# Kernel tuning notes

Measured on AMD Instinct MI355X. Metric: run time of the kernel, lower is better.

Reference implementation:

```python
import jax, jax.numpy as jnp
import numpy as np

N_NODES = 100000
N_EDGES = 1280000
IN_CH = 64
OUT_CH = 64


def setup_inputs() -> dict:
    key = jax.random.key(0)
    k1, k2, k3, k4 = jax.random.split(key, 4)
    x = jax.random.normal(k1, (N_NODES, IN_CH), dtype=jnp.float32)
    edge_index = jax.random.randint(k2, (2, N_EDGES), 0, N_NODES, dtype=jnp.int64)
    # GraphConv params (glorot weight, zero bias)
    scale = jnp.sqrt(6.0 / (IN_CH + OUT_CH)).astype(jnp.float32)
    W = jax.random.uniform(k3, (IN_CH, OUT_CH), dtype=jnp.float32, minval=-scale, maxval=scale)
    b = jnp.zeros((OUT_CH,), dtype=jnp.float32)
    return {"x": x, "edge_index": edge_index, "W": W, "b": b}


def reference(x, edge_index, W, b):
    # DGL GraphConv, norm='both': out = D_in^{-1/2} A^T (D_out^{-1/2} x W) + b
    src, dst = edge_index[0], edge_index[1]
    ones = jnp.ones((src.shape[0],), dtype=x.dtype)
    out_deg = jax.ops.segment_sum(ones, src, num_segments=N_NODES)
    in_deg = jax.ops.segment_sum(ones, dst, num_segments=N_NODES)
    norm_src = jnp.where(out_deg > 0, jax.lax.rsqrt(jnp.maximum(out_deg, 1.0)), 0.0)
    norm_dst = jnp.where(in_deg > 0, jax.lax.rsqrt(jnp.maximum(in_deg, 1.0)), 0.0)
    # in_feats <= out_feats: transform first, then aggregate
    h = (x * norm_src[:, None]) @ W              # [N, OUT_CH]
    msg = h[src]                                 # gather  [E, OUT_CH]
    agg = jax.ops.segment_sum(msg, dst, num_segments=N_NODES)  # scatter-add [N, OUT_CH]
    return agg * norm_dst[:, None] + b
```

## Files before the change

kernel.cpp:

```cpp
#include <hip/hip_runtime.h>
#include <hip/hip_fp16.h>

#define CH 64
#define CAP 40
#define SPILLMAX 4096
#define RANGE 12500
#define SLICES 64
#define TILE 2048
#define EPT 8
#define BSH 9
#define BKT 512

__global__ __launch_bounds__(256) void hist_kernel(const int* __restrict__ src,
                                                   unsigned short* __restrict__ partial,
                                                   int E, int N, int R)
{
    __shared__ int h[RANGE];
    int r  = blockIdx.x % R;
    int sl = blockIdx.x / R;
    int lo = r * RANGE;
    int hi = min(lo + RANGE, N);
    int span = hi - lo;
    for (int i = threadIdx.x; i < span; i += 256) h[i] = 0;
    __syncthreads();
    int per = (E + SLICES - 1) / SLICES;
    int sb = sl * per, se = min(sb + per, E);
    for (int e = sb + threadIdx.x * 4; e < se; e += 256 * 4) {
        if (e + 4 <= se) {
            int4 v = *(const int4*)(src + e);
            if (v.x >= lo && v.x < hi) atomicAdd(&h[v.x - lo], 1);
            if (v.y >= lo && v.y < hi) atomicAdd(&h[v.y - lo], 1);
            if (v.z >= lo && v.z < hi) atomicAdd(&h[v.z - lo], 1);
            if (v.w >= lo && v.w < hi) atomicAdd(&h[v.w - lo], 1);
        } else {
            for (int k = e; k < se; ++k) {
                int sv = src[k];
                if (sv >= lo && sv < hi) atomicAdd(&h[sv - lo], 1);
            }
        }
    }
    __syncthreads();
    unsigned short* pp = partial + (size_t)blockIdx.x * RANGE;
    for (int i = threadIdx.x; i < span; i += 256) pp[i] = (unsigned short)h[i];
}

__global__ __launch_bounds__(256) void rpscale_kernel(const unsigned short* __restrict__ partial,
                                                      const float* __restrict__ x,
                                                      __half* __restrict__ xh, int N, int R)
{
    __shared__ float nsl[256];
    int tid = threadIdx.x;
    int n0 = blockIdx.x * 256;
    int n = n0 + tid;
    if (n < N) {
        int r = n / RANGE, off = n - r * RANGE;
        int s = 0;
        #pragma unroll 8
        for (int sl = 0; sl < SLICES; ++sl)
            s += partial[(size_t)(sl * R + r) * RANGE + off];
        nsl[tid] = (s > 0) ? rsqrtf((float)s) : 0.0f;
    } else {
        nsl[tid] = 0.0f;
    }
    __syncthreads();
    int sub = tid & 7;
    int nl0 = tid >> 3;
    for (int p = 0; p < 8; ++p) {
        int nl = p * 32 + nl0;
        int node = n0 + nl;
        if (node >= N) break;
        float ns = nsl[nl];
        const float4* xp = (const float4*)(x + (size_t)node * CH + sub * 8);
        float4 a = xp[0], b = xp[1];
        __half2 h0 = __floats2half2_rn(a.x * ns, a.y * ns);
        __half2 h1 = __floats2half2_rn(a.z * ns, a.w * ns);
        __half2 h2 = __floats2half2_rn(b.x * ns, b.y * ns);
        __half2 h3 = __floats2half2_rn(b.z * ns, b.w * ns);
        uint4 u;
        u.x = (unsigned)__half_as_ushort(h0.x) | ((unsigned)__half_as_ushort(h0.y) << 16);
        u.y = (unsigned)__half_as_ushort(h1.x) | ((unsigned)__half_as_ushort(h1.y) << 16);
        u.z = (unsigned)__half_as_ushort(h2.x) | ((unsigned)__half_as_ushort(h2.y) << 16);
        u.w = (unsigned)__half_as_ushort(h3.x) | ((unsigned)__half_as_ushort(h3.y) << 16);
        *(uint4*)(xh + (size_t)node * CH + sub * 8) = u;
    }
}

__global__ __launch_bounds__(256) void binA_kernel(const int* __restrict__ dst,
                                                   int* __restrict__ tileHist,
                                                   int* __restrict__ nspill, int E)
{
    if (blockIdx.x == 0 && threadIdx.x == 0) nspill[0] = 0;
    __shared__ int h[256];
    int tid = threadIdx.x;
    int t = blockIdx.x;
    h[tid] = 0;
    __syncthreads();
    int e0 = t * TILE + tid * EPT;
    if (e0 + EPT <= E) {
        const int4* dp = (const int4*)(dst + e0);
        int4 a = dp[0], b = dp[1];
        atomicAdd(&h[a.x >> BSH], 1); atomicAdd(&h[a.y >> BSH], 1);
        atomicAdd(&h[a.z >> BSH], 1); atomicAdd(&h[a.w >> BSH], 1);
        atomicAdd(&h[b.x >> BSH], 1); atomicAdd(&h[b.y >> BSH], 1);
        atomicAdd(&h[b.z >> BSH], 1); atomicAdd(&h[b.w >> BSH], 1);
    } else {
        for (int k = e0; k < E && k < e0 + EPT; ++k) atomicAdd(&h[dst[k] >> BSH], 1);
    }
    __syncthreads();
    tileHist[t * 256 + tid] = h[tid];
}

__global__ __launch_bounds__(256) void binB_kernel(int* __restrict__ tileHist,
                                                   int* __restrict__ totals, int NT)
{
    __shared__ int sm[256];
    int b = blockIdx.x, tid = threadIdx.x;
    int C = (NT + 255) / 256;
    int vals[8];
    int s = 0;
    for (int k = 0; k < C; ++k) {
        int t = tid * C + k;
        vals[k] = (t < NT) ? tileHist[t * 256 + b] : 0;
        s += vals[k];
    }
    sm[tid] = s;
    __syncthreads();
    for (int d = 1; d < 256; d <<= 1) {
        int v = (tid >= d) ? sm[tid - d] : 0;
        __syncthreads();
        sm[tid] += v;
        __syncthreads();
    }
    int off = (tid > 0) ? sm[tid - 1] : 0;
    for (int k = 0; k < C; ++k) {
        int t = tid * C + k;
        if (t < NT) { tileHist[t * 256 + b] = off; off += vals[k]; }
    }
    if (tid == 255) totals[b] = sm[255];
}

__global__ __launch_bounds__(256) void binC_kernel(const int* __restrict__ src,
                                                   const int* __restrict__ dst,
                                                   const int* __restrict__ tileBase,
                                                   const int* __restrict__ totals,
                                                   int* __restrict__ sorted, int E, int NB)
{
    __shared__ int sm[256];
    __shared__ int cur[256];
    int tid = threadIdx.x;
    int t = blockIdx.x;
    sm[tid] = (tid < NB) ? totals[tid] : 0;
    __syncthreads();
    for (int d = 1; d < 256; d <<= 1) {
        int v = (tid >= d) ? sm[tid - d] : 0;
        __syncthreads();
        sm[tid] += v;
        __syncthreads();
    }
    int bb = (tid > 0) ? sm[tid - 1] : 0;
    cur[tid] = (tid < NB) ? bb + tileBase[t * 256 + tid] : 0;
    __syncthreads();
    int e0 = t * TILE + tid * EPT;
    int s[EPT], d[EPT];
    int nk = 0;
    if (e0 + EPT <= E) {
        const int4* sp = (const int4*)(src + e0);
        const int4* dp = (const int4*)(dst + e0);
        int4 a = sp[0], b = sp[1], c = dp[0], f = dp[1];
        s[0]=a.x; s[1]=a.y; s[2]=a.z; s[3]=a.w; s[4]=b.x; s[5]=b.y; s[6]=b.z; s[7]=b.w;
        d[0]=c.x; d[1]=c.y; d[2]=c.z; d[3]=c.w; d[4]=f.x; d[5]=f.y; d[6]=f.z; d[7]=f.w;
        nk = EPT;
    } else {
        for (int k = 0; e0 + k < E && k < EPT; ++k) { s[k] = src[e0+k]; d[k] = dst[e0+k]; nk++; }
    }
    for (int k = 0; k < nk; ++k) {
        int p = d[k] >> BSH;
        int pos = atomicAdd(&cur[p], 1);
        sorted[pos] = (s[k] << BSH) | (d[k] & (BKT - 1));
    }
}

__global__ __launch_bounds__(256) void binD_kernel(const int* __restrict__ sorted,
                                                   const int* __restrict__ totals,
                                                   int* __restrict__ bucket,
                                                   int* __restrict__ cnt,
                                                   int* __restrict__ spill,
                                                   int* __restrict__ nspill, int N, int NB)
{
    __shared__ int sm[256];
    __shared__ int lc[BKT];
    int b = blockIdx.x, tid = threadIdx.x;
    sm[tid] = (tid < NB) ? totals[tid] : 0;
    lc[tid] = 0; lc[tid + 256] = 0;
    __syncthreads();
    for (int d = 1; d < 256; d <<= 1) {
        int v = (tid >= d) ? sm[tid - d] : 0;
        __syncthreads();
        sm[tid] += v;
        __syncthreads();
    }
    int beg = (b > 0) ? sm[b - 1] : 0;
    int end = sm[b];
    int nbase = b << BSH;
    for (int i = beg + tid; i < end; i += 256) {
        int v = sorted[i];
        int sv = v >> BSH;
        int dl = v & (BKT - 1);
        int pos = atomicAdd(&lc[dl], 1);
        if (pos < CAP) {
            bucket[(size_t)(nbase + dl) * CAP + pos] = sv;
        } else {
            int sp = atomicAdd(nspill, 1);
            if (sp < SPILLMAX) { spill[2*sp] = nbase + dl; spill[2*sp+1] = sv; }
        }
    }
    __syncthreads();
    int n0 = nbase + tid;
    if (n0 < N) cnt[n0] = lc[tid];
    int n1 = nbase + 256 + tid;
    if (n1 < N) cnt[n1] = lc[256 + tid];
}

__global__ __launch_bounds__(256) void agg_kernel(const __half* __restrict__ xh,
                                                  const int* __restrict__ bucket,
                                                  const int* __restrict__ cnt,
                                                  const int* __restrict__ spill,
                                                  const int* __restrict__ nspill,
                                                  __half* __restrict__ aggh, int N)
{
    int node = (blockIdx.x * blockDim.x + threadIdx.x) >> 5;
    int sl = threadIdx.x & 31;
    if (node >= N) return;
    int c = cnt[node];
    int m = (c < CAP) ? c : CAP;
    const int* bp = bucket + (size_t)node * CAP;
    float ax0 = 0, ay0 = 0, ax1 = 0, ay1 = 0, ax2 = 0, ay2 = 0, ax3 = 0, ay3 = 0;
    int j = 0;
    for (; j + 8 <= m; j += 8) {
        int4 va = *(const int4*)(bp + j);
        int4 vb = *(const int4*)(bp + j + 4);
        float2 f0 = __half22float2(*(const __half2*)(xh + (size_t)va.x * CH + sl * 2));
        float2 f1 = __half22float2(*(const __half2*)(xh + (size_t)va.y * CH + sl * 2));
        float2 f2 = __half22float2(*(const __half2*)(xh + (size_t)va.z * CH + sl * 2));
        float2 f3 = __half22float2(*(const __half2*)(xh + (size_t)va.w * CH + sl * 2));
        float2 f4 = __half22float2(*(const __half2*)(xh + (size_t)vb.x * CH + sl * 2));
        float2 f5 = __half22float2(*(const __half2*)(xh + (size_t)vb.y * CH + sl * 2));
        float2 f6 = __half22float2(*(const __half2*)(xh + (size_t)vb.z * CH + sl * 2));
        float2 f7 = __half22float2(*(const __half2*)(xh + (size_t)vb.w * CH + sl * 2));
        ax0 += f0.x + f4.x; ay0 += f0.y + f4.y;
        ax1 += f1.x + f5.x; ay1 += f1.y + f5.y;
        ax2 += f2.x + f6.x; ay2 += f2.y + f6.y;
        ax3 += f3.x + f7.x; ay3 += f3.y + f7.y;
    }
    for (; j + 4 <= m; j += 4) {
        int4 va = *(const int4*)(bp + j);
        float2 f0 = __half22float2(*(const __half2*)(xh + (size_t)va.x * CH + sl * 2));
        float2 f1 = __half22float2(*(const __half2*)(xh + (size_t)va.y * CH + sl * 2));
        float2 f2 = __half22float2(*(const __half2*)(xh + (size_t)va.z * CH + sl * 2));
        float2 f3 = __half22float2(*(const __half2*)(xh + (size_t)va.w * CH + sl * 2));
        ax0 += f0.x; ay0 += f0.y;
        ax1 += f1.x; ay1 += f1.y;
        ax2 += f2.x; ay2 += f2.y;
        ax3 += f3.x; ay3 += f3.y;
    }
    for (; j < m; ++j) {
        float2 f = __half22float2(*(const __half2*)(xh + (size_t)bp[j] * CH + sl * 2));
        ax0 += f.x; ay0 += f.y;
    }
    if (c > CAP) {
        int ns = *nspill;
        if (ns > SPILLMAX) ns = SPILLMAX;
        for (int i = 0; i < ns; ++i) {
            if (spill[2 * i] == node) {
                float2 f = __half22float2(*(const __half2*)(xh + (size_t)spill[2 * i + 1] * CH + sl * 2));
                ax0 += f.x; ay0 += f.y;
            }
        }
    }
    float nd = (c > 0) ? rsqrtf((float)c) : 0.0f;
    float rx = ((ax0 + ax1) + (ax2 + ax3)) * nd;
    float ry = ((ay0 + ay1) + (ay2 + ay3)) * nd;
    *(__half2*)(aggh + (size_t)node * CH + sl * 2) = __floats2half2_rn(rx, ry);
}

__global__ __launch_bounds__(256) void gemm_out_kernel(const __half* __restrict__ aggh,
                                                       const float* __restrict__ W,
                                                       const float* __restrict__ bias,
                                                       float* __restrict__ out, int N)
{
    int g = blockIdx.x * 256 + threadIdx.x;
    int waveId = __builtin_amdgcn_readfirstlane(g >> 6);
    int lane = threadIdx.x & 63;
    int quarter = waveId & 3;
    int row = ((waveId >> 2) << 6) + lane;
    if (row >= N) return;
    const int cbase = quarter * 16;
    float acc[16];
    #pragma unroll
    for (int i = 0; i < 16; ++i) acc[i] = 0.0f;
    const __half* xp = aggh + (size_t)row * CH;
    for (int k0 = 0; k0 < CH; k0 += 8) {
        uint4 u = *(const uint4*)(xp + k0);
        const __half2* hp = (const __half2*)&u;
        float xk[8];
        #pragma unroll
        for (int j = 0; j < 4; ++j) {
            float2 f = __half22float2(hp[j]);
            xk[2 * j] = f.x; xk[2 * j + 1] = f.y;
        }
        #pragma unroll
        for (int kk = 0; kk < 8; ++kk) {
            const float* wrow = W + (k0 + kk) * CH + cbase;
            #pragma unroll
            for (int q = 0; q < 4; ++q) {
                float4 w = *(const float4*)(wrow + q * 4);
                acc[q * 4 + 0] += xk[kk] * w.x;
                acc[q * 4 + 1] += xk[kk] * w.y;
                acc[q * 4 + 2] += xk[kk] * w.z;
                acc[q * 4 + 3] += xk[kk] * w.w;
            }
        }
    }
    float* op = out + (size_t)row * CH + cbase;
    #pragma unroll
    for (int q = 0; q < 4; ++q) {
        float4 b = *(const float4*)(bias + cbase + q * 4);
        float4 o;
        o.x = acc[q * 4 + 0] + b.x;
        o.y = acc[q * 4 + 1] + b.y;
        o.z = acc[q * 4 + 2] + b.z;
        o.w = acc[q * 4 + 3] + b.w;
        *(float4*)(op + q * 4) = o;
    }
}

extern "C" void kernel_launch(void* const* d_in, const int* in_sizes, int n_in,
                              void* d_out, int out_size, void* d_ws, size_t ws_size,
                              hipStream_t stream)
{
    const float* x    = (const float*)d_in[0];
    const int*   edge = (const int*)d_in[1];
    const float* W    = (const float*)d_in[2];
    const float* bias = (const float*)d_in[3];
    float* out = (float*)d_out;

    int N = in_sizes[0] / CH;
    int E = in_sizes[1] / 2;
    const int* src = edge;
    const int* dst = edge + E;
    int R  = (N + RANGE - 1) / RANGE;
    int NT = (E + TILE - 1) / TILE;
    int NB = (N + BKT - 1) >> BSH;

    int* nspill  = (int*)d_ws;
    int* spill   = nspill + 64;
    int* cnt     = spill + 2 * SPILLMAX;
    int* bucket  = cnt + N;
    unsigned short* partial = (unsigned short*)(bucket + (size_t)N * CAP);
    int* tileHist = (int*)partial;
    int* totals   = tileHist + NT * 256;
    int* sorted   = totals + 320;
    size_t psz = (size_t)SLICES * R * RANGE * sizeof(unsigned short);
    size_t osz = (size_t)(NT * 256 + 320 + E) * sizeof(int);
    size_t xoff = ((((char*)partial - (char*)d_ws) + (psz > osz ? psz : osz)) + 255) & ~(size_t)255;
    __half* xh = (__half*)((char*)d_ws + xoff);
    size_t aoff = ((xoff + (size_t)N * CH * sizeof(__half)) + 255) & ~(size_t)255;
    __half* aggh = (__half*)((char*)d_ws + aoff);

    hist_kernel<<<R * SLICES, 256, 0, stream>>>(src, partial, E, N, R);
    rpscale_kernel<<<(N + 255) / 256, 256, 0, stream>>>(partial, x, xh, N, R);
    binA_kernel<<<NT, 256, 0, stream>>>(dst, tileHist, nspill, E);
    binB_kernel<<<NB, 256, 0, stream>>>(tileHist, totals, NT);
    binC_kernel<<<NT, 256, 0, stream>>>(src, dst, tileHist, totals, sorted, E, NB);
    binD_kernel<<<NB, 256, 0, stream>>>(sorted, totals, bucket, cnt, spill, nspill, N, NB);
    agg_kernel<<<((size_t)N * 32 + 255) / 256, 256, 0, stream>>>(xh, bucket, cnt, spill,
                                                                 nspill, aggh, N);
    int nwaves = 4 * ((N + 63) / 64);
    gemm_out_kernel<<<(nwaves + 3) / 4, 256, 0, stream>>>(aggh, W, bias, out, N);
}
```

Before: 114.0 us.

## Merge histogram and binning kernels into combined launches via block-index dispatch

Combines the source-degree histogram with the destination tile histogram into one launch, and the rpscale/normalisation kernel with the bucket prefix-scan kernel into another, dispatching on block index. This removes two kernel launches and lets independent work run concurrently on the GPU. The workspace layout is reorganised so tileHist no longer aliases the partial buffer, and CAP shrinks from 40 to 32, which may push more nodes into the spill path. The tile-histogram blocks now allocate the large 12500-int shared array, which can reduce occupancy for those blocks.

```diff
diff --git a/kernel.cpp b/kernel.cpp
--- a/kernel.cpp
+++ b/kernel.cpp
@@ -2,7 +2,7 @@
 #include <hip/hip_fp16.h>
 
 #define CH 64
-#define CAP 40
+#define CAP 32
 #define SPILLMAX 4096
 #define RANGE 12500
 #define SLICES 64
@@ -11,132 +11,134 @@
 #define BSH 9
 #define BKT 512
 
-__global__ __launch_bounds__(256) void hist_kernel(const int* __restrict__ src,
-                                                   unsigned short* __restrict__ partial,
-                                                   int E, int N, int R)
+__global__ __launch_bounds__(256) void histA_kernel(const int* __restrict__ src,
+                                                    const int* __restrict__ dst,
+                                                    unsigned short* __restrict__ partial,
+                                                    int* __restrict__ tileHist,
+                                                    int* __restrict__ nspill,
+                                                    int E, int N, int R, int NT)
 {
     __shared__ int h[RANGE];
-    int r  = blockIdx.x % R;
-    int sl = blockIdx.x / R;
-    int lo = r * RANGE;
-    int hi = min(lo + RANGE, N);
-    int span = hi - lo;
-    for (int i = threadIdx.x; i < span; i += 256) h[i] = 0;
-    __syncthreads();
-    int per = (E + SLICES - 1) / SLICES;
-    int sb = sl * per, se = min(sb + per, E);
-    for (int e = sb + threadIdx.x * 4; e < se; e += 256 * 4) {
-        if (e + 4 <= se) {
-            int4 v = *(const int4*)(src + e);
-            if (v.x >= lo && v.x < hi) atomicAdd(&h[v.x - lo], 1);
-            if (v.y >= lo && v.y < hi) atomicAdd(&h[v.y - lo], 1);
-            if (v.z >= lo && v.z < hi) atomicAdd(&h[v.z - lo], 1);
-            if (v.w >= lo && v.w < hi) atomicAdd(&h[v.w - lo], 1);
+    int tid = threadIdx.x;
+    int bid = blockIdx.x;
+    if (bid < NT) {
+        if (bid == 0 && tid == 0) nspill[0] = 0;
+        h[tid] = 0;
+        __syncthreads();
+        int e0 = bid * TILE + tid * EPT;
+        if (e0 + EPT <= E) {
+            const int4* dp = (const int4*)(dst + e0);
+            int4 a = dp[0], b = dp[1];
+            atomicAdd(&h[a.x >> BSH], 1); atomicAdd(&h[a.y >> BSH], 1);
+            atomicAdd(&h[a.z >> BSH], 1); atomicAdd(&h[a.w >> BSH], 1);
+            atomicAdd(&h[b.x >> BSH], 1); atomicAdd(&h[b.y >> BSH], 1);
+            atomicAdd(&h[b.z >> BSH], 1); atomicAdd(&h[b.w >> BSH], 1);
         } else {
-            for (int k = e; k < se; ++k) {
-                int sv = src[k];
-                if (sv >= lo && sv < hi) atomicAdd(&h[sv - lo], 1);
+            for (int k = e0; k < E && k < e0 + EPT; ++k) atomicAdd(&h[dst[k] >> BSH], 1);
+        }
+        __syncthreads();
+        tileHist[bid * 256 + tid] = h[tid];
+    } else {
+        int hb = bid - NT;
+        int r  = hb % R;
+        int sl = hb / R;
+        int lo = r * RANGE;
+        int hi = min(lo + RANGE, N);
+        int span = hi - lo;
+        for (int i = tid; i < span; i += 256) h[i] = 0;
+        __syncthreads();
+        int per = (E + SLICES - 1) / SLICES;
+        int sb = sl * per, se = min(sb + per, E);
+        for (int e = sb + tid * 4; e < se; e += 256 * 4) {
+            if (e + 4 <= se) {
+                int4 v = *(const int4*)(src + e);
+                if (v.x >= lo && v.x < hi) atomicAdd(&h[v.x - lo], 1);
+                if (v.y >= lo && v.y < hi) atomicAdd(&h[v.y - lo], 1);
+                if (v.z >= lo && v.z < hi) atomicAdd(&h[v.z - lo], 1);
+                if (v.w >= lo && v.w < hi) atomicAdd(&h[v.w - lo], 1);
+            } else {
+                for (int k = e; k < se; ++k) {
+                    int sv = src[k];
+                    if (sv >= lo && sv < hi) atomicAdd(&h[sv - lo], 1);
+                }
             }
         }
-    }
-    __syncthreads();
-    unsigned short* pp = partial + (size_t)blockIdx.x * RANGE;
-    for (int i = threadIdx.x; i < span; i += 256) pp[i] = (unsigned short)h[i];
-}
-
-__global__ __launch_bounds__(256) void rpscale_kernel(const unsigned short* __restrict__ partial,
-                                                      const float* __restrict__ x,
-                                                      __half* __restrict__ xh, int N, int R)
+        __syncthreads();
+        unsigned short* pp = partial + (size_t)hb * RANGE;
+        for (int i = tid; i < span; i += 256) pp[i] = (unsigned short)h[i];
+    }
+}
+
+__global__ __launch_bounds__(256) void rpscaleB_kernel(const unsigned short* __restrict__ partial,
+                                                       const float* __restrict__ x,
+                                                       __half* __restrict__ xh,
+                                                       int* __restrict__ tileHist,
+                                                       int* __restrict__ totals,
+                                                       int N, int R, int NT, int NPB)
 {
     __shared__ float nsl[256];
+    __shared__ int sm[256];
     int tid = threadIdx.x;
-    int n0 = blockIdx.x * 256;
-    int n = n0 + tid;
-    if (n < N) {
-        int r = n / RANGE, off = n - r * RANGE;
+    int bid = blockIdx.x;
+    if (bid < NPB) {
+        int n0 = bid * 256;
+        int n = n0 + tid;
+        if (n < N) {
+            int r = n / RANGE, off = n - r * RANGE;
+            int s = 0;
+            #pragma unroll 8
+            for (int sl = 0; sl < SLICES; ++sl)
+                s += partial[(size_t)(sl * R + r) * RANGE + off];
+            nsl[tid] = (s > 0) ? rsqrtf((float)s) : 0.0f;
+        } else {
+            nsl[tid] = 0.0f;
+        }
+        __syncthreads();
+        int sub = tid & 7;
+        int nl0 = tid >> 3;
+        for (int p = 0; p < 8; ++p) {
+            int nl = p * 32 + nl0;
+            int node = n0 + nl;
+            if (node >= N) break;
+            float ns = nsl[nl];
+            const float4* xp = (const float4*)(x + (size_t)node * CH + sub * 8);
+            float4 a = xp[0], b = xp[1];
+            __half2 h0 = __floats2half2_rn(a.x * ns, a.y * ns);
+            __half2 h1 = __floats2half2_rn(a.z * ns, a.w * ns);
+            __half2 h2 = __floats2half2_rn(b.x * ns, b.y * ns);
+            __half2 h3 = __floats2half2_rn(b.z * ns, b.w * ns);
+            uint4 u;
+            u.x = (unsigned)__half_as_ushort(h0.x) | ((unsigned)__half_as_ushort(h0.y) << 16);
+            u.y = (unsigned)__half_as_ushort(h1.x) | ((unsigned)__half_as_ushort(h1.y) << 16);
+            u.z = (unsigned)__half_as_ushort(h2.x) | ((unsigned)__half_as_ushort(h2.y) << 16);
+            u.w = (unsigned)__half_as_ushort(h3.x) | ((unsigned)__half_as_ushort(h3.y) << 16);
+            *(uint4*)(xh + (size_t)node * CH + sub * 8) = u;
+        }
+    } else {
+        int b = bid - NPB;
+        int C = (NT + 255) / 256;
+        int vals[8];
         int s = 0;
-        #pragma unroll 8
-        for (int sl = 0; sl < SLICES; ++sl)
-            s += partial[(size_t)(sl * R + r) * RANGE + off];
-        nsl[tid] = (s > 0) ? rsqrtf((float)s) : 0.0f;
-    } else {
-        nsl[tid] = 0.0f;
-    }
-    __syncthreads();
-    int sub = tid & 7;
-    int nl0 = tid >> 3;
-    for (int p = 0; p < 8; ++p) {
-        int nl = p * 32 + nl0;
-        int node = n0 + nl;
-        if (node >= N) break;
-        float ns = nsl[nl];
-        const float4* xp = (const float4*)(x + (size_t)node * CH + sub * 8);
-        float4 a = xp[0], b = xp[1];
-        __half2 h0 = __floats2half2_rn(a.x * ns, a.y * ns);
-        __half2 h1 = __floats2half2_rn(a.z * ns, a.w * ns);
-        __half2 h2 = __floats2half2_rn(b.x * ns, b.y * ns);
-        __half2 h3 = __floats2half2_rn(b.z * ns, b.w * ns);
-        uint4 u;
-        u.x = (unsigned)__half_as_ushort(h0.x) | ((unsigned)__half_as_ushort(h0.y) << 16);
-        u.y = (unsigned)__half_as_ushort(h1.x) | ((unsigned)__half_as_ushort(h1.y) << 16);
-        u.z = (unsigned)__half_as_ushort(h2.x) | ((unsigned)__half_as_ushort(h2.y) << 16);
-        u.w = (unsigned)__half_as_ushort(h3.x) | ((unsigned)__half_as_ushort(h3.y) << 16);
-        *(uint4*)(xh + (size_t)node * CH + sub * 8) = u;
-    }
-}
-
-__global__ __launch_bounds__(256) void binA_kernel(const int* __restrict__ dst,
-                                                   int* __restrict__ tileHist,
-                                                   int* __restrict__ nspill, int E)
-{
-    if (blockIdx.x == 0 && threadIdx.x == 0) nspill[0] = 0;
-    __shared__ int h[256];
-    int tid = threadIdx.x;
-    int t = blockIdx.x;
-    h[tid] = 0;
-    __syncthreads();
-    int e0 = t * TILE + tid * EPT;
-    if (e0 + EPT <= E) {
-        const int4* dp = (const int4*)(dst + e0);
-        int4 a = dp[0], b = dp[1];
-        atomicAdd(&h[a.x >> BSH], 1); atomicAdd(&h[a.y >> BSH], 1);
-        atomicAdd(&h[a.z >> BSH], 1); atomicAdd(&h[a.w >> BSH], 1);
-        atomicAdd(&h[b.x >> BSH], 1); atomicAdd(&h[b.y >> BSH], 1);
-        atomicAdd(&h[b.z >> BSH], 1); atomicAdd(&h[b.w >> BSH], 1);
-    } else {
-        for (int k = e0; k < E && k < e0 + EPT; ++k) atomicAdd(&h[dst[k] >> BSH], 1);
-    }
-    __syncthreads();
-    tileHist[t * 256 + tid] = h[tid];
-}
-
-__global__ __launch_bounds__(256) void binB_kernel(int* __restrict__ tileHist,
-                                                   int* __restrict__ totals, int NT)
-{
-    __shared__ int sm[256];
-    int b = blockIdx.x, tid = threadIdx.x;
-    int C = (NT + 255) / 256;
-    int vals[8];
-    int s = 0;
-    for (int k = 0; k < C; ++k) {
-        int t = tid * C + k;
-        vals[k] = (t < NT) ? tileHist[t * 256 + b] : 0;
-        s += vals[k];
-    }
-    sm[tid] = s;
-    __syncthreads();
-    for (int d = 1; d < 256; d <<= 1) {
-        int v = (tid >= d) ? sm[tid - d] : 0;
-        __syncthreads();
-        sm[tid] += v;
-        __syncthreads();
-    }
-    int off = (tid > 0) ? sm[tid - 1] : 0;
-    for (int k = 0; k < C; ++k) {
-        int t = tid * C + k;
-        if (t < NT) { tileHist[t * 256 + b] = off; off += vals[k]; }
-    }
-    if (tid == 255) totals[b] = sm[255];
+        for (int k = 0; k < C; ++k) {
+            int t = tid * C + k;
+            vals[k] = (t < NT) ? tileHist[t * 256 + b] : 0;
+            s += vals[k];
+        }
+        sm[tid] = s;
+        __syncthreads();
+        for (int d = 1; d < 256; d <<= 1) {
+            int v = (tid >= d) ? sm[tid - d] : 0;
+            __syncthreads();
+            sm[tid] += v;
+            __syncthreads();
+        }
+        int off = (tid > 0) ? sm[tid - 1] : 0;
+        for (int k = 0; k < C; ++k) {
+            int t = tid * C + k;
+            if (t < NT) { tileHist[t * 256 + b] = off; off += vals[k]; }
+        }
+        if (tid == 255) totals[b] = sm[255];
+    }
 }
 
 __global__ __launch_bounds__(256) void binC_kernel(const int* __restrict__ src,
@@ -348,29 +350,29 @@
     int E = in_sizes[1] / 2;
     const int* src = edge;
     const int* dst = edge + E;
-    int R  = (N + RANGE - 1) / RANGE;
-    int NT = (E + TILE - 1) / TILE;
-    int NB = (N + BKT - 1) >> BSH;
+    int R   = (N + RANGE - 1) / RANGE;
+    int NT  = (E + TILE - 1) / TILE;
+    int NB  = (N + BKT - 1) >> BSH;
+    int NPB = (N + 255) / 256;
 
     int* nspill  = (int*)d_ws;
     int* spill   = nspill + 64;
     int* cnt     = spill + 2 * SPILLMAX;
     int* bucket  = cnt + N;
     unsigned short* partial = (unsigned short*)(bucket + (size_t)N * CAP);
-    int* tileHist = (int*)partial;
+    int* tileHist = (int*)(partial + (size_t)SLICES * R * RANGE);
     int* totals   = tileHist + NT * 256;
-    int* sorted   = totals + 320;
-    size_t psz = (size_t)SLICES * R * RANGE * sizeof(unsigned short);
-    size_t osz = (size_t)(NT * 256 + 320 + E) * sizeof(int);
-    size_t xoff = ((((char*)partial - (char*)d_ws) + (psz > osz ? psz : osz)) + 255) & ~(size_t)255;
+    int* sorted   = (int*)partial;
+    size_t endoff = (char*)(totals + 320) - (char*)d_ws;
+    size_t xoff = (endoff + 255) & ~(size_t)255;
     __half* xh = (__half*)((char*)d_ws + xoff);
     size_t aoff = ((xoff + (size_t)N * CH * sizeof(__half)) + 255) & ~(size_t)255;
     __half* aggh = (__half*)((char*)d_ws + aoff);
 
-    hist_kernel<<<R * SLICES, 256, 0, stream>>>(src, partial, E, N, R);
-    rpscale_kernel<<<(N + 255) / 256, 256, 0, stream>>>(partial, x, xh, N, R);
-    binA_kernel<<<NT, 256, 0, stream>>>(dst, tileHist, nspill, E);
-    binB_kernel<<<NB, 256, 0, stream>>>(tileHist, totals, NT);
+    histA_kernel<<<NT + R * SLICES, 256, 0, stream>>>(src, dst, partial, tileHist,
+                                                      nspill, E, N, R, NT);
+    rpscaleB_kernel<<<NPB + NB, 256, 0, stream>>>(partial, x, xh, tileHist, totals,
+                                                  N, R, NT, NPB);
     binC_kernel<<<NT, 256, 0, stream>>>(src, dst, tileHist, totals, sorted, E, NB);
     binD_kernel<<<NB, 256, 0, stream>>>(sorted, totals, bucket, cnt, spill, nspill, N, NB);
     agg_kernel<<<((size_t)N * 32 + 255) / 256, 256, 0, stream>>>(xh, bucket, cnt, spill,
```

Measured after the change: 109.7 us. 3.7% less time.
